# Optimization experiments

Measured on AMD Instinct MI355X. Metric: run time of the kernel, lower is better.

## Reference

```python
import jax, jax.numpy as jnp
import numpy as np

S, N, CM, CZ, H, D = 512, 768, 64, 128, 8, 32
EPS = 1e-5


def _layer_norm(x, w, b):
    mu = jnp.mean(x, axis=-1, keepdims=True)
    xc = x - mu
    var = jnp.mean(xc * xc, axis=-1, keepdims=True)
    return xc * jax.lax.rsqrt(var + EPS) * w + b


def setup_inputs() -> dict:
    key = jax.random.key(0)
    ks = jax.random.split(key, 6)
    scale_m = 1.0 / np.sqrt(CM)
    scale_z = 1.0 / np.sqrt(CZ)
    scale_o = 1.0 / np.sqrt(H * D)
    return {
        "m": jax.random.normal(ks[0], (1, S, N, CM), jnp.float32),
        "z": jax.random.normal(ks[1], (1, N, N, CZ), jnp.float32),
        "norm_m_w": jnp.ones((CM,), jnp.float32),
        "norm_m_b": jnp.zeros((CM,), jnp.float32),
        "norm_z_w": jnp.ones((CZ,), jnp.float32),
        "norm_z_b": jnp.zeros((CZ,), jnp.float32),
        "wm": jax.random.normal(ks[2], (CM, H * D), jnp.float32) * scale_m,
        "wg": jax.random.normal(ks[3], (CM, H * D), jnp.float32) * scale_m,
        "wz": jax.random.normal(ks[4], (CZ, H), jnp.float32) * scale_z,
        "wo": jax.random.normal(ks[5], (H * D, CM), jnp.float32) * scale_o,
    }


def reference(m, z, norm_m_w, norm_m_b, norm_z_w, norm_z_b, wm, wg, wz, wo):
    m0 = m[0]  # [S, N, CM]
    z0 = z[0]  # [N, N, CZ]
    mn = _layer_norm(m0, norm_m_w, norm_m_b)
    zn = _layer_norm(z0, norm_z_w, norm_z_b)
    # b[p,q,h]; original code softmaxes over the LAST axis of b'[h,p,q] (axis q)
    # but contracts as o[s,q] = sum_p w[p,q] v[s,p] (transpose_a matmul),
    # so softmax is over axis q = axis 1 of [p,q,h].
    b = jnp.einsum('pqc,ch->pqh', zn, wz)
    w = jax.nn.softmax(b, axis=1)  # normalized over q for each p (faithful to source)
    v = jnp.einsum('spc,ck->spk', mn, wm).reshape(S, N, H, D)
    g = jax.nn.sigmoid(jnp.einsum('spc,ck->spk', mn, wg)).reshape(S, N, H, D)
    o = jnp.einsum('pqh,sphd->sqhd', w, v) * g  # weighted average then gate
    out = jnp.einsum('sqhd,hdc->sqc', o, wo.reshape(H, D, CM))
    return out[None]  # [1, S, N, CM]
```

## Files before the change

### kernel.cpp

```cpp
#include <hip/hip_runtime.h>
#include <hip/hip_bf16.h>
#include <stdint.h>

#define S_DIM 512
#define N_DIM 768
#define CMd   64
#define CZd   128
#define Hd    8
#define Dd    32
#define HDd   256

typedef float          f32x4  __attribute__((ext_vector_type(4)));
typedef __bf16         bf16x8 __attribute__((ext_vector_type(8)));
typedef unsigned int   u32x4  __attribute__((ext_vector_type(4)));
typedef unsigned int   u32x2  __attribute__((ext_vector_type(2)));
typedef unsigned short u16x8  __attribute__((ext_vector_type(8)));

__device__ __forceinline__ unsigned short f2bf(float f) {
  __bf16 h = (__bf16)f;
  return __builtin_bit_cast(unsigned short, h);
}
__device__ __forceinline__ float bf2f(unsigned short u) {
  unsigned int x = ((unsigned int)u) << 16;
  return __builtin_bit_cast(float, x);
}
__device__ __forceinline__ float sigmoidf_(float x) {
  return 1.f / (1.f + __expf(-x));
}

typedef __attribute__((address_space(1))) const void cg_void;
typedef __attribute__((address_space(3))) void lds_void;
__device__ __forceinline__ void async16(const unsigned short* g, unsigned short* l) {
  __builtin_amdgcn_global_load_lds((cg_void*)g, (lds_void*)l, 16, 0, 0);
}

__global__ __launch_bounds__(256) void k0_prep(const float* __restrict__ wm,
                                               const float* __restrict__ wg,
                                               const float* __restrict__ wo,
                                               unsigned short* __restrict__ WBT,
                                               unsigned short* __restrict__ woT) {
  int t = blockIdx.x * 256 + threadIdx.x;
  if (t < 512 * 64) {
    int j = t >> 6, c = t & 63;
    float v = (j < 256) ? wm[c * 256 + j] : wg[c * 256 + (j - 256)];
    WBT[t] = f2bf(v);
  }
  if (t < 64 * 256) {
    int c = t >> 8, k = t & 255;
    woT[t] = f2bf(wo[k * 64 + c]);
  }
}

__global__ __launch_bounds__(256) void k1_zln_b(const float* __restrict__ z,
                                                const float* __restrict__ nzw,
                                                const float* __restrict__ nzb,
                                                const float* __restrict__ wz,
                                                float* __restrict__ b_e) {
  __shared__ float wzT[8][128];
  int t = threadIdx.x;
  for (int i = t; i < 1024; i += 256) {
    int h = i >> 7, c = i & 127;
    wzT[h][c] = wz[c * 8 + h];
  }
  __syncthreads();

  int lane = t & 63, w = t >> 6;
  int sub = lane & 7;
  int rloc = lane >> 3;
  int p = blockIdx.y;
  int q = blockIdx.x * 32 + w * 8 + rloc;

  const float* zr = z + ((size_t)p * N_DIM + q) * CZd + sub * 16;
  f32x4 v[4];
#pragma unroll
  for (int j = 0; j < 4; j++) v[j] = *(const f32x4*)(zr + 4 * j);

  float s1 = 0.f, s2 = 0.f;
#pragma unroll
  for (int j = 0; j < 4; j++)
#pragma unroll
    for (int e = 0; e < 4; e++) { float x = v[j][e]; s1 += x; s2 += x * x; }
  s1 += __shfl_xor(s1, 1); s2 += __shfl_xor(s2, 1);
  s1 += __shfl_xor(s1, 2); s2 += __shfl_xor(s2, 2);
  s1 += __shfl_xor(s1, 4); s2 += __shfl_xor(s2, 4);
  float mean = s1 * (1.f / 128.f);
  float var  = s2 * (1.f / 128.f) - mean * mean;
  float rstd = rsqrtf(var + 1e-5f);

  const float* wp = nzw + sub * 16;
  const float* bp = nzb + sub * 16;
  float zn[16];
#pragma unroll
  for (int j = 0; j < 4; j++) {
    f32x4 wv = *(const f32x4*)(wp + 4 * j);
    f32x4 bv = *(const f32x4*)(bp + 4 * j);
#pragma unroll
    for (int e = 0; e < 4; e++)
      zn[j * 4 + e] = (v[j][e] - mean) * rstd * wv[e] + bv[e];
  }

  float accb[8];
#pragma unroll
  for (int h = 0; h < 8; h++) {
    const f32x4* wr = (const f32x4*)&wzT[h][sub * 16];
    float a = 0.f;
#pragma unroll
    for (int j = 0; j < 4; j++) {
      f32x4 ww = wr[j];
#pragma unroll
      for (int e = 0; e < 4; e++) a += zn[j * 4 + e] * ww[e];
    }
    accb[h] = a;
  }
#pragma unroll
  for (int mask = 1; mask <= 4; mask <<= 1)
#pragma unroll
    for (int h = 0; h < 8; h++) accb[h] += __shfl_xor(accb[h], mask);

  float outv = accb[0];
#pragma unroll
  for (int h = 1; h < 8; h++) outv = (sub == h) ? accb[h] : outv;
  b_e[((size_t)p * 8 + sub) * 768 + q] = outv;
}

__global__ __launch_bounds__(256) void k1b_softmax(float* __restrict__ b_e,
                                                   float* __restrict__ invs) {
  int row = blockIdx.x;
  int t = threadIdx.x;
  float* base = b_e + (size_t)row * 768;
  float x0 = base[t], x1 = base[t + 256], x2 = base[t + 512];
  __shared__ float red[256];
  red[t] = fmaxf(x0, fmaxf(x1, x2));
  __syncthreads();
  for (int o = 128; o > 0; o >>= 1) {
    if (t < o) red[t] = fmaxf(red[t], red[t + o]);
    __syncthreads();
  }
  float M = red[0];
  __syncthreads();
  float e0 = __expf(x0 - M), e1 = __expf(x1 - M), e2 = __expf(x2 - M);
  base[t] = e0; base[t + 256] = e1; base[t + 512] = e2;
  red[t] = e0 + e1 + e2;
  __syncthreads();
  for (int o = 128; o > 0; o >>= 1) {
    if (t < o) red[t] += red[t + o];
    __syncthreads();
  }
  if (t == 0) invs[row] = 1.0f / red[0];
}

__global__ __launch_bounds__(256) void k1b2_transpose(const float* __restrict__ b_e,
                                                      const float* __restrict__ invs,
                                                      unsigned short* __restrict__ Aw) {
  int t = threadIdx.x;
  int q0 = blockIdx.x * 64, p0 = blockIdx.y * 64, h = blockIdx.z;
  __shared__ unsigned short T[64][65];
  int i = t >> 2, ch = t & 3;
  size_t rowid = (size_t)(p0 + i) * 8 + h;
  const float* src = b_e + rowid * 768 + q0 + ch * 16;
  float inv = invs[rowid];
#pragma unroll
  for (int jj = 0; jj < 16; jj += 4) {
    f32x4 v = *(const f32x4*)(src + jj);
#pragma unroll
    for (int e = 0; e < 4; e++) T[i][ch * 16 + jj + e] = f2bf(v[e] * inv);
  }
  __syncthreads();
  int j = i;
  unsigned short outv[16];
#pragma unroll
  for (int ii = 0; ii < 16; ii++) outv[ii] = T[ch * 16 + ii][j];
  int rx = (j & 7) << 3;
  unsigned short* dstrow = Aw + ((size_t)h * 768 + q0 + j) * 768 + p0;
  *(u32x4*)(dstrow + ((ch * 16) ^ rx))     = *(u32x4*)(outv);
  *(u32x4*)(dstrow + ((ch * 16 + 8) ^ rx)) = *(u32x4*)(outv + 8);
}

__global__ __launch_bounds__(256) void k2_mln_vg(const float* __restrict__ mp,
                                                 const float* __restrict__ nmw,
                                                 const float* __restrict__ nmb,
                                                 const unsigned short* __restrict__ WBT,
                                                 unsigned short* __restrict__ VT,
                                                 unsigned short* __restrict__ G) {
  __shared__ unsigned short WBs[512 * 64];
  __shared__ unsigned short As[64 * 64];
  int t = threadIdx.x;
  int p0 = blockIdx.x * 64, s = blockIdx.y;

#pragma unroll
  for (int it = 0; it < 16; it++) {
    int cid = t + it * 256;
    int row = cid >> 3, ch = cid & 7;
    u32x4 v = *(const u32x4*)(WBT + row * 64 + ch * 8);
    *(u32x4*)(WBs + row * 64 + ((ch * 8) ^ ((row & 7) << 3))) = v;
  }

  {
    int row = t >> 2, qt = t & 3;
    const float* mr = mp + ((size_t)s * N_DIM + p0 + row) * CMd + qt * 16;
    f32x4 v[4];
#pragma unroll
    for (int j = 0; j < 4; j++) v[j] = *(const f32x4*)(mr + 4 * j);
    float s1 = 0.f, s2 = 0.f;
#pragma unroll
    for (int j = 0; j < 4; j++)
#pragma unroll
      for (int e = 0; e < 4; e++) { float x = v[j][e]; s1 += x; s2 += x * x; }
    s1 += __shfl_xor(s1, 1); s2 += __shfl_xor(s2, 1);
    s1 += __shfl_xor(s1, 2); s2 += __shfl_xor(s2, 2);
    float mean = s1 * (1.f / 64.f);
    float var  = s2 * (1.f / 64.f) - mean * mean;
    float rstd = rsqrtf(var + 1e-5f);
    unsigned short o[16];
#pragma unroll
    for (int j = 0; j < 4; j++) {
      f32x4 wv = *(const f32x4*)(nmw + qt * 16 + 4 * j);
      f32x4 bv = *(const f32x4*)(nmb + qt * 16 + 4 * j);
#pragma unroll
      for (int e = 0; e < 4; e++)
        o[j * 4 + e] = f2bf((v[j][e] - mean) * rstd * wv[e] + bv[e]);
    }
    int k0 = qt * 16;
    *(u32x4*)(As + row * 64 + ((k0) ^ ((row & 7) << 3)))     = *(u32x4*)(o);
    *(u32x4*)(As + row * 64 + ((k0 + 8) ^ ((row & 7) << 3))) = *(u32x4*)(o + 8);
  }
  __syncthreads();

  int lane = t & 63, w = t >> 6;
  int n0 = w * 128;
  int lr = lane & 15, lk8 = (lane >> 4) * 8;
  f32x4 zero = {0.f, 0.f, 0.f, 0.f};
  f32x4 acc[4][8];
#pragma unroll
  for (int i = 0; i < 4; i++)
#pragma unroll
    for (int j = 0; j < 8; j++) acc[i][j] = zero;

#pragma unroll
  for (int kk = 0; kk < 2; kk++) {
    bf16x8 bfr[8];
#pragma unroll
    for (int nt = 0; nt < 8; nt++) {
      int r = n0 + nt * 16 + lr;
      bfr[nt] = *(const bf16x8*)(WBs + r * 64 + ((kk * 32 + lk8) ^ ((r & 7) << 3)));
    }
#pragma unroll
    for (int mt = 0; mt < 4; mt++) {
      int ar = mt * 16 + lr;
      bf16x8 a = *(const bf16x8*)(As + ar * 64 + ((kk * 32 + lk8) ^ ((ar & 7) << 3)));
#pragma unroll
      for (int nt = 0; nt < 8; nt++)
        acc[mt][nt] = __builtin_amdgcn_mfma_f32_16x16x32_bf16(a, bfr[nt], acc[mt][nt], 0, 0, 0);
    }
  }

#pragma unroll
  for (int mt = 0; mt < 4; mt++)
#pragma unroll
    for (int nt = 0; nt < 8; nt++) {
      int j = n0 + nt * 16 + lr;
      int ploc = mt * 16 + (lane >> 4) * 4;
      if (j < 256) {
        int h = j >> 5, d = j & 31;
        unsigned short pk[4];
#pragma unroll
        for (int r = 0; r < 4; r++) pk[r] = f2bf(acc[mt][nt][r]);
        int pswz = ((((ploc >> 3) ^ (lr & 7)) << 3) | (ploc & 7));
        *(u32x2*)(VT + ((size_t)h * 16384 + s * 32 + d) * 768 + p0 + pswz) = *(u32x2*)pk;
      } else {
        int jj = j - 256;
#pragma unroll
        for (int r = 0; r < 4; r++)
          G[((size_t)s * 768 + p0 + ploc + r) * 256 + jj] = f2bf(sigmoidf_(acc[mt][nt][r]));
      }
    }
}

__global__ __launch_bounds__(256) void k34_fused(const unsigned short* __restrict__ Aw,
                                                 const unsigned short* __restrict__ VT,
                                                 const unsigned short* __restrict__ G,
                                                 const unsigned short* __restrict__ woT,
                                                 float* __restrict__ out) {
  __shared__ unsigned short Asl[2][128 * 64];
  __shared__ unsigned short Bsl[2][64 * 64];
  int t = threadIdx.x;
  int flat = blockIdx.x;
  int xcd = flat & 7, idx = flat >> 3;
  int n_idx = xcd * 32 + idx / 6;
  int q_idx = idx % 6;
  int q0 = q_idx * 128, n0 = n_idx * 64;
  int s0 = n0 >> 5;

  int lane = t & 63, w = t >> 6;
  int wq = w >> 1, wn = w & 1;
  int wr = wq * 64;
  int wc = wn * 32;
  int lr = lane & 15, lg = lane >> 4;

  const size_t aOff = (size_t)(q0 + w * 32 + (lane >> 3)) * 768 + (lane & 7) * 8;
  const size_t bOff = (size_t)(n0 + w * 16 + (lane >> 3)) * 768 + (lane & 7) * 8;

  auto STAGE = [&](int h, int kt, int buf) {
    const unsigned short* a = Aw + (size_t)h * 589824 + aOff + kt * 64;
    const unsigned short* b = VT + (size_t)h * 12582912 + bOff + kt * 64;
    unsigned short* la = &Asl[buf][w * 2048];
    unsigned short* lb = &Bsl[buf][w * 1024];
#pragma unroll
    for (int i = 0; i < 4; i++) async16(a + (size_t)i * 6144, la + i * 512);
#pragma unroll
    for (int i = 0; i < 2; i++) async16(b + (size_t)i * 6144, lb + i * 512);
  };

  f32x4 zero = {0.f, 0.f, 0.f, 0.f};
  f32x4 oh[4][2];
  f32x4 oc[4][4];
#pragma unroll
  for (int i = 0; i < 4; i++) {
#pragma unroll
    for (int j = 0; j < 2; j++) oh[i][j] = zero;
#pragma unroll
    for (int j = 0; j < 4; j++) oc[i][j] = zero;
  }

  STAGE(0, 0, 0);
  asm volatile("s_waitcnt vmcnt(0)" ::: "memory");
  __builtin_amdgcn_sched_barrier(0);
  __syncthreads();

  for (int h = 0; h < 8; h++) {
    for (int kt = 0; kt < 12; kt++) {
      int cur = kt & 1;
      if (kt < 11)      STAGE(h, kt + 1, cur ^ 1);
      else if (h < 7)   STAGE(h + 1, 0, cur ^ 1);
#pragma unroll
      for (int kk = 0; kk < 2; kk++) {
        int kc = kk * 32 + lg * 8;
        bf16x8 af[4], bfv[2];
#pragma unroll
        for (int i = 0; i < 4; i++) {
          int arr = wr + i * 16 + lr;
          af[i] = *(const bf16x8*)(&Asl[cur][arr * 64 + (kc ^ ((arr & 7) << 3))]);
        }
#pragma unroll
        for (int j = 0; j < 2; j++) {
          int brr = wc + j * 16 + lr;
          bfv[j] = *(const bf16x8*)(&Bsl[cur][brr * 64 + (kc ^ ((brr & 7) << 3))]);
        }
#pragma unroll
        for (int mt = 0; mt < 4; mt++)
#pragma unroll
          for (int nt = 0; nt < 2; nt++)
            oh[mt][nt] = __builtin_amdgcn_mfma_f32_16x16x32_bf16(af[mt], bfv[nt], oh[mt][nt], 0, 0, 0);
      }
      asm volatile("s_waitcnt vmcnt(0)" ::: "memory");
      __builtin_amdgcn_sched_barrier(0);
      __syncthreads();
    }

    unsigned short* slab = &Asl[1][w * 2048];
    int sg = s0 + wn;
#pragma unroll
    for (int mt = 0; mt < 4; mt++)
#pragma unroll
      for (int nt = 0; nt < 2; nt++) {
        int d = nt * 16 + lr;
        int qg = q0 + wr + mt * 16 + lg * 4;
        const unsigned short* gp = G + ((size_t)sg * 768 + qg) * 256 + h * 32 + d;
#pragma unroll
        for (int r = 0; r < 4; r++) {
          float g = bf2f(gp[(size_t)r * 256]);
          int ql = mt * 16 + lg * 4 + r;
          slab[ql * 32 + (d ^ ((ql & 3) << 3))] = f2bf(oh[mt][nt][r] * g);
          oh[mt][nt][r] = 0.f;
        }
      }
    asm volatile("s_waitcnt lgkmcnt(0)" ::: "memory");
    __builtin_amdgcn_sched_barrier(0);
    bf16x8 pa[4];
#pragma unroll
    for (int mq = 0; mq < 4; mq++) {
      int ql = mq * 16 + lr;
      pa[mq] = *(const bf16x8*)(slab + ql * 32 + ((lg * 8) ^ ((ql & 3) << 3)));
    }
#pragma unroll
    for (int nc = 0; nc < 4; nc++) {
      bf16x8 wb = *(const bf16x8*)(woT + (size_t)(nc * 16 + lr) * 256 + h * 32 + lg * 8);
#pragma unroll
      for (int mq = 0; mq < 4; mq++)
        oc[mq][nc] = __builtin_amdgcn_mfma_f32_16x16x32_bf16(pa[mq], wb, oc[mq][nc], 0, 0, 0);
    }
    asm volatile("s_waitcnt lgkmcnt(0)" ::: "memory");
    __builtin_amdgcn_sched_barrier(0);
  }

  int sg = s0 + wn;
#pragma unroll
  for (int mq = 0; mq < 4; mq++)
#pragma unroll
    for (int nc = 0; nc < 4; nc++) {
      int c = nc * 16 + lr;
      int qg = q0 + wr + mq * 16 + lg * 4;
      float* dst = out + ((size_t)sg * 768 + qg) * 64 + c;
#pragma unroll
      for (int r = 0; r < 4; r++) dst[(size_t)r * 64] = oc[mq][nc][r];
    }
}

extern "C" void kernel_launch(void* const* d_in, const int* in_sizes, int n_in,
                              void* d_out, int out_size, void* d_ws, size_t ws_size,
                              hipStream_t stream) {
  const float* m   = (const float*)d_in[0];
  const float* z   = (const float*)d_in[1];
  const float* nmw = (const float*)d_in[2];
  const float* nmb = (const float*)d_in[3];
  const float* nzw = (const float*)d_in[4];
  const float* nzb = (const float*)d_in[5];
  const float* wm  = (const float*)d_in[6];
  const float* wg  = (const float*)d_in[7];
  const float* wz  = (const float*)d_in[8];
  const float* wo  = (const float*)d_in[9];
  float* out = (float*)d_out;

  char* ws = (char*)d_ws;
  size_t off = 0;
  auto alloc = [&](size_t bytes) -> void* {
    void* p = ws + off;
    off += (bytes + 1023) & ~(size_t)1023;
    return p;
  };
  float*          b_e  = (float*)alloc((size_t)768 * 8 * 768 * 4);
  float*          invs = (float*)alloc((size_t)768 * 8 * 4);
  unsigned short* Awt  = (unsigned short*)alloc((size_t)8 * 768 * 768 * 2);
  unsigned short* WBT  = (unsigned short*)alloc((size_t)512 * 64 * 2);
  unsigned short* woT  = (unsigned short*)alloc((size_t)64 * 256 * 2);
  unsigned short* VT   = (unsigned short*)alloc((size_t)8 * 16384 * 768 * 2);
  unsigned short* G    = (unsigned short*)alloc((size_t)512 * 768 * 256 * 2);
  if (ws_size < off) return;

  k0_prep<<<128, 256, 0, stream>>>(wm, wg, wo, WBT, woT);
  k1_zln_b<<<dim3(24, 768), 256, 0, stream>>>(z, nzw, nzb, wz, b_e);
  k1b_softmax<<<6144, 256, 0, stream>>>(b_e, invs);
  k1b2_transpose<<<dim3(12, 12, 8), 256, 0, stream>>>(b_e, invs, Awt);
  k2_mln_vg<<<dim3(12, 512), 256, 0, stream>>>(m, nmw, nmb, WBT, VT, G);
  k34_fused<<<dim3(1536), 256, 0, stream>>>(Awt, VT, G, woT, out);
}
```

Before: 757.7 us.

## Retile fused attention-output kernel to single-buffer 64q x 128n tiles with occupancy hint

Restructures the fused weighted-average and output-projection kernel. Each block now covers 64 q rows by 128 (s,d) columns, and each wave owns one s slice. Double-buffered LDS staging is replaced with a single buffer that loads synchronously, and the gated slab moves to its own padded LDS region. A launch bound of 3 blocks per CU is added so more blocks can reside and hide latency in place of the removed software prefetch. In exchange, memory loads no longer overlap compute within a block, and the wider blocks reduce how much each A tile is reused.

```diff
diff --git a/kernel.cpp b/kernel.cpp
--- a/kernel.cpp
+++ b/kernel.cpp
@@ -276,40 +276,28 @@
     }
 }
 
-__global__ __launch_bounds__(256) void k34_fused(const unsigned short* __restrict__ Aw,
-                                                 const unsigned short* __restrict__ VT,
-                                                 const unsigned short* __restrict__ G,
-                                                 const unsigned short* __restrict__ woT,
-                                                 float* __restrict__ out) {
-  __shared__ unsigned short Asl[2][128 * 64];
-  __shared__ unsigned short Bsl[2][64 * 64];
+__global__ __launch_bounds__(256, 3) void k34_fused(const unsigned short* __restrict__ Aw,
+                                                    const unsigned short* __restrict__ VT,
+                                                    const unsigned short* __restrict__ G,
+                                                    const unsigned short* __restrict__ woT,
+                                                    float* __restrict__ out) {
+  __shared__ unsigned short Asl[64 * 64];
+  __shared__ unsigned short Bsl[128 * 64];
+  __shared__ unsigned short SLAB[4 * 64 * 40];
+
   int t = threadIdx.x;
   int flat = blockIdx.x;
-  int xcd = flat & 7, idx = flat >> 3;
-  int n_idx = xcd * 32 + idx / 6;
-  int q_idx = idx % 6;
-  int q0 = q_idx * 128, n0 = n_idx * 64;
-  int s0 = n0 >> 5;
+  int g = (flat & 7) * 192 + (flat >> 3);
+  int q_t = g >> 7, n_t = g & 127;
+  int q0 = q_t * 64, n0 = n_t * 128;
 
   int lane = t & 63, w = t >> 6;
-  int wq = w >> 1, wn = w & 1;
-  int wr = wq * 64;
-  int wc = wn * 32;
   int lr = lane & 15, lg = lane >> 4;
-
-  const size_t aOff = (size_t)(q0 + w * 32 + (lane >> 3)) * 768 + (lane & 7) * 8;
-  const size_t bOff = (size_t)(n0 + w * 16 + (lane >> 3)) * 768 + (lane & 7) * 8;
-
-  auto STAGE = [&](int h, int kt, int buf) {
-    const unsigned short* a = Aw + (size_t)h * 589824 + aOff + kt * 64;
-    const unsigned short* b = VT + (size_t)h * 12582912 + bOff + kt * 64;
-    unsigned short* la = &Asl[buf][w * 2048];
-    unsigned short* lb = &Bsl[buf][w * 1024];
-#pragma unroll
-    for (int i = 0; i < 4; i++) async16(a + (size_t)i * 6144, la + i * 512);
-#pragma unroll
-    for (int i = 0; i < 2; i++) async16(b + (size_t)i * 6144, lb + i * 512);
-  };
+  int s_w = n_t * 4 + w;
+
+  const size_t aOff = (size_t)(q0 + w * 16 + (lane >> 3)) * 768 + (lane & 7) * 8;
+  const size_t bOff = (size_t)(n0 + w * 32 + (lane >> 3)) * 768 + (lane & 7) * 8;
+  unsigned short* slab = SLAB + w * 2560;
 
   f32x4 zero = {0.f, 0.f, 0.f, 0.f};
   f32x4 oh[4][2];
@@ -322,85 +310,86 @@
     for (int j = 0; j < 4; j++) oc[i][j] = zero;
   }
 
-  STAGE(0, 0, 0);
-  asm volatile("s_waitcnt vmcnt(0)" ::: "memory");
-  __builtin_amdgcn_sched_barrier(0);
-  __syncthreads();
-
+#pragma unroll 1
   for (int h = 0; h < 8; h++) {
+    const unsigned short* Ah = Aw + (size_t)h * 589824;
+    const unsigned short* Bh = VT + (size_t)h * 12582912;
+
+#pragma unroll 1
     for (int kt = 0; kt < 12; kt++) {
-      int cur = kt & 1;
-      if (kt < 11)      STAGE(h, kt + 1, cur ^ 1);
-      else if (h < 7)   STAGE(h + 1, 0, cur ^ 1);
-#pragma unroll
-      for (int kk = 0; kk < 2; kk++) {
-        int kc = kk * 32 + lg * 8;
-        bf16x8 af[4], bfv[2];
-#pragma unroll
-        for (int i = 0; i < 4; i++) {
-          int arr = wr + i * 16 + lr;
-          af[i] = *(const bf16x8*)(&Asl[cur][arr * 64 + (kc ^ ((arr & 7) << 3))]);
-        }
-#pragma unroll
-        for (int j = 0; j < 2; j++) {
-          int brr = wc + j * 16 + lr;
-          bfv[j] = *(const bf16x8*)(&Bsl[cur][brr * 64 + (kc ^ ((brr & 7) << 3))]);
-        }
-#pragma unroll
-        for (int mt = 0; mt < 4; mt++)
-#pragma unroll
-          for (int nt = 0; nt < 2; nt++)
-            oh[mt][nt] = __builtin_amdgcn_mfma_f32_16x16x32_bf16(af[mt], bfv[nt], oh[mt][nt], 0, 0, 0);
-      }
+      int ko = kt * 64;
+#pragma unroll
+      for (int i = 0; i < 2; i++)
+        async16(Ah + aOff + (size_t)i * 8 * 768 + ko, Asl + w * 1024 + i * 512);
+#pragma unroll
+      for (int i = 0; i < 4; i++)
+        async16(Bh + bOff + (size_t)i * 8 * 768 + ko, Bsl + w * 2048 + i * 512);
       asm volatile("s_waitcnt vmcnt(0)" ::: "memory");
       __builtin_amdgcn_sched_barrier(0);
       __syncthreads();
-    }
-
-    unsigned short* slab = &Asl[1][w * 2048];
-    int sg = s0 + wn;
-#pragma unroll
-    for (int mt = 0; mt < 4; mt++)
-#pragma unroll
-      for (int nt = 0; nt < 2; nt++) {
-        int d = nt * 16 + lr;
-        int qg = q0 + wr + mt * 16 + lg * 4;
-        const unsigned short* gp = G + ((size_t)sg * 768 + qg) * 256 + h * 32 + d;
+#pragma unroll
+      for (int kk = 0; kk < 2; kk++) {
+        int kc = kk * 32 + lg * 8;
+        bf16x8 afr[4], bfr[2];
+#pragma unroll
+        for (int mq = 0; mq < 4; mq++) {
+          int ar = mq * 16 + lr;
+          afr[mq] = *(const bf16x8*)(Asl + ar * 64 + (kc ^ ((ar & 7) << 3)));
+        }
+#pragma unroll
+        for (int j = 0; j < 2; j++) {
+          int br = w * 32 + j * 16 + lr;
+          bfr[j] = *(const bf16x8*)(Bsl + br * 64 + (kc ^ ((br & 7) << 3)));
+        }
+#pragma unroll
+        for (int mq = 0; mq < 4; mq++)
+#pragma unroll
+          for (int j = 0; j < 2; j++)
+            oh[mq][j] = __builtin_amdgcn_mfma_f32_16x16x32_bf16(afr[mq], bfr[j], oh[mq][j], 0, 0, 0);
+      }
+      __syncthreads();
+    }
+
+    asm volatile("s_waitcnt lgkmcnt(0)" ::: "memory");
+    __builtin_amdgcn_sched_barrier(0);
+
+#pragma unroll
+    for (int mq = 0; mq < 4; mq++)
+#pragma unroll
+      for (int j = 0; j < 2; j++) {
+        int d = j * 16 + lr;
+        const unsigned short* gp =
+            G + ((size_t)s_w * 768 + q0 + mq * 16 + lg * 4) * 256 + h * 32 + d;
 #pragma unroll
         for (int r = 0; r < 4; r++) {
-          float g = bf2f(gp[(size_t)r * 256]);
-          int ql = mt * 16 + lg * 4 + r;
-          slab[ql * 32 + (d ^ ((ql & 3) << 3))] = f2bf(oh[mt][nt][r] * g);
-          oh[mt][nt][r] = 0.f;
+          float gv = bf2f(gp[(size_t)r * 256]);
+          int ql = mq * 16 + lg * 4 + r;
+          slab[ql * 40 + d] = f2bf(oh[mq][j][r] * gv);
+          oh[mq][j][r] = 0.f;
         }
       }
     asm volatile("s_waitcnt lgkmcnt(0)" ::: "memory");
     __builtin_amdgcn_sched_barrier(0);
-    bf16x8 pa[4];
-#pragma unroll
-    for (int mq = 0; mq < 4; mq++) {
-      int ql = mq * 16 + lr;
-      pa[mq] = *(const bf16x8*)(slab + ql * 32 + ((lg * 8) ^ ((ql & 3) << 3)));
-    }
+
+    bf16x8 pa[4], wb[4];
+#pragma unroll
+    for (int mq = 0; mq < 4; mq++)
+      pa[mq] = *(const bf16x8*)(slab + (mq * 16 + lr) * 40 + lg * 8);
+#pragma unroll
+    for (int nc = 0; nc < 4; nc++)
+      wb[nc] = *(const bf16x8*)(woT + (size_t)(nc * 16 + lr) * 256 + h * 32 + lg * 8);
+#pragma unroll
+    for (int mq = 0; mq < 4; mq++)
+#pragma unroll
+      for (int nc = 0; nc < 4; nc++)
+        oc[mq][nc] = __builtin_amdgcn_mfma_f32_16x16x32_bf16(pa[mq], wb[nc], oc[mq][nc], 0, 0, 0);
+  }
+
+#pragma unroll
+  for (int mq = 0; mq < 4; mq++)
 #pragma unroll
     for (int nc = 0; nc < 4; nc++) {
-      bf16x8 wb = *(const bf16x8*)(woT + (size_t)(nc * 16 + lr) * 256 + h * 32 + lg * 8);
-#pragma unroll
-      for (int mq = 0; mq < 4; mq++)
-        oc[mq][nc] = __builtin_amdgcn_mfma_f32_16x16x32_bf16(pa[mq], wb, oc[mq][nc], 0, 0, 0);
-    }
-    asm volatile("s_waitcnt lgkmcnt(0)" ::: "memory");
-    __builtin_amdgcn_sched_barrier(0);
-  }
-
-  int sg = s0 + wn;
-#pragma unroll
-  for (int mq = 0; mq < 4; mq++)
-#pragma unroll
-    for (int nc = 0; nc < 4; nc++) {
-      int c = nc * 16 + lr;
-      int qg = q0 + wr + mq * 16 + lg * 4;
-      float* dst = out + ((size_t)sg * 768 + qg) * 64 + c;
+      float* dst = out + ((size_t)s_w * 768 + q0 + mq * 16 + lg * 4) * 64 + nc * 16 + lr;
 #pragma unroll
       for (int r = 0; r < 4; r++) dst[(size_t)r * 64] = oc[mq][nc][r];
     }
```

Result: faster. 735.3 us (-3.0%).
